# Performance work log

Hardware: AMD Instinct MI355X
Metric: run time of the kernel (lower is better)

## Reference

```python
import jax, jax.numpy as jnp
import numpy as np

B, Q, K, D, H, HD, OUT = 4, 1024, 1024, 256, 8, 32, 256


def setup_inputs() -> dict:
    key = jax.random.key(0)
    ks = jax.random.split(key, 11)
    s = 0.05  # small init scale for weights
    return {
        "q_data": jax.random.normal(ks[0], (B, Q, D), jnp.float32),
        "m_data": jax.random.normal(ks[1], (B, K, D), jnp.float32),
        "bias": jax.random.normal(ks[2], (B, 1, 1, K), jnp.float32),
        "nonbatched_bias": jax.random.normal(ks[3], (H, Q, K), jnp.float32),
        "query_w": jax.random.normal(ks[4], (D, H, HD), jnp.float32) * s,
        "key_w": jax.random.normal(ks[5], (D, H, HD), jnp.float32) * s,
        "value_w": jax.random.normal(ks[6], (D, H, HD), jnp.float32) * s,
        "gating_w": jax.random.normal(ks[7], (D, H, HD), jnp.float32) * s,
        "gating_b": jnp.ones((H, HD), jnp.float32),
        "output_w": jax.random.normal(ks[8], (H, HD, OUT), jnp.float32) * s,
        "output_b": jnp.zeros((OUT,), jnp.float32),
    }


def reference(q_data, m_data, bias, nonbatched_bias, query_w, key_w, value_w,
              gating_w, gating_b, output_w, output_b):
    key_dim = query_w.shape[-1]
    # QKV projections; queries pre-scaled by 1/sqrt(head_dim)
    q = jnp.einsum('bqa,ahc->bqhc', q_data, query_w) * key_dim ** (-0.5)
    k = jnp.einsum('bka,ahc->bkhc', m_data, key_w)
    v = jnp.einsum('bka,ahc->bkhc', m_data, value_w)
    # attention logits [b,h,q,k] plus batched and nonbatched additive biases
    logits_update = jnp.einsum('bqhc,bkhc->bhqk', q, k)
    logits = logits_update + bias + nonbatched_bias[None]
    weights = jax.nn.softmax(logits, axis=-1)
    weighted_avg = jnp.einsum('bhqk,bkhc->bqhc', weights, v)
    # sigmoid gating on the value-aggregated output
    gate = jax.nn.sigmoid(jnp.einsum('bqc,chv->bqhv', q_data, gating_w) + gating_b)
    weighted_avg = weighted_avg * gate
    output = jnp.einsum('bqhc,hco->bqo', weighted_avg, output_w) + output_b
    return (output, logits_update)
```

## Files before the change

### kernel.cpp

```cpp
#include <hip/hip_runtime.h>
#include <hip/hip_bf16.h>

#define NB 4
#define NQ 1024
#define NKS 1024
#define ND 256
#define NH 8
#define NHD 32
#define NOUT 256

typedef __attribute__((ext_vector_type(8))) short v8s;
typedef __attribute__((ext_vector_type(4))) short v4s;
typedef __attribute__((ext_vector_type(4))) float f32x4;

__global__ __launch_bounds__(256) void prep_all(
    const float* __restrict__ qd, const float* __restrict__ md,
    const float* __restrict__ qw, const float* __restrict__ kw,
    const float* __restrict__ vw, const float* __restrict__ gw,
    const float* __restrict__ ow,
    __hip_bfloat16* __restrict__ Abf, __hip_bfloat16* __restrict__ Wt)
{
  if (blockIdx.x < 1024) {
    const int gid = blockIdx.x * 256 + threadIdx.x;
    const float* src = (gid < 131072) ? qd : md;
    const size_t off = (size_t)(gid & 131071) * 8;
    const float4 a = ((const float4*)(src + off))[0];
    const float4 c = ((const float4*)(src + off))[1];
    __hip_bfloat16 t8[8];
    t8[0]=__float2bfloat16(a.x); t8[1]=__float2bfloat16(a.y);
    t8[2]=__float2bfloat16(a.z); t8[3]=__float2bfloat16(a.w);
    t8[4]=__float2bfloat16(c.x); t8[5]=__float2bfloat16(c.y);
    t8[6]=__float2bfloat16(c.z); t8[7]=__float2bfloat16(c.w);
    *(v8s*)(Abf + (size_t)gid * 8) = *(v8s*)t8;
    return;
  }
  __shared__ float tile[64][65];
  const int wb = blockIdx.x - 1024;
  const int m = wb >> 4, bx = wb & 15;
  const float* src = (m == 0) ? qw : (m == 1) ? kw : (m == 2) ? vw
                   : (m == 3) ? gw : ow;
  const float scale = (m == 0) ? 0.1767766952966369f : 1.0f;
  const int d0 = (bx >> 2) * 64, o0 = (bx & 3) * 64;
  #pragma unroll
  for (int i = 0; i < 16; ++i) {
    const int idx = threadIdx.x + i * 256;
    tile[idx >> 6][idx & 63] = src[(size_t)(d0 + (idx >> 6)) * 256 + o0 + (idx & 63)];
  }
  __syncthreads();
  __hip_bfloat16* dst = Wt + (size_t)m * 65536;
  #pragma unroll
  for (int i = 0; i < 16; ++i) {
    const int idx = threadIdx.x + i * 256;
    const int orow = idx >> 6, dc = idx & 63;
    dst[(size_t)(o0 + orow) * 256 + d0 + dc] = __float2bfloat16(tile[dc][orow] * scale);
  }
}

__global__ __launch_bounds__(256) void proj_kernel(
    const __hip_bfloat16* __restrict__ Abf, const __hip_bfloat16* __restrict__ Wt,
    const float* __restrict__ gating_b,
    __hip_bfloat16* __restrict__ Qw, __hip_bfloat16* __restrict__ Kw,
    __hip_bfloat16* __restrict__ Vt, __hip_bfloat16* __restrict__ G)
{
  const int wv = threadIdx.x >> 6, lane = threadIdx.x & 63;
  const int c = lane & 15, g = lane >> 4;
  const int task = blockIdx.x * 4 + wv;
  const int ctg = task & 3;
  const int mat = (task >> 2) & 1;
  const int r0g = (task >> 3) & 255;
  const int src = task >> 11;
  const int r0 = r0g * 16;
  const int b = r0 >> 10, pos0 = r0 & 1023;
  const f32x4 z = {0.f, 0.f, 0.f, 0.f};

  const __hip_bfloat16* A = Abf + ((size_t)src * 4096 + r0) * 256;
  v8s af[8];
  #pragma unroll
  for (int ks = 0; ks < 8; ++ks)
    af[ks] = *(const v8s*)(A + c * 256 + ks * 32 + g * 8);

  const int widx = (src == 0) ? (mat ? 3 : 0) : (mat ? 2 : 1);
  const __hip_bfloat16* W = Wt + (size_t)widx * 65536;
  const bool swapped = (src == 1) && (mat == 1);

  f32x4 ac[4] = {z, z, z, z};
  #pragma unroll
  for (int ks = 0; ks < 8; ++ks) {
    #pragma unroll
    for (int j = 0; j < 4; ++j) {
      v8s wf = *(const v8s*)(W + (size_t)((ctg * 4 + j) * 16 + c) * 256 + ks * 32 + g * 8);
      ac[j] = swapped
        ? __builtin_amdgcn_mfma_f32_16x16x32_bf16(wf, af[ks], ac[j], 0, 0, 0)
        : __builtin_amdgcn_mfma_f32_16x16x32_bf16(af[ks], wf, ac[j], 0, 0, 0);
    }
  }

  if (src == 0 && mat == 0) {
    #pragma unroll
    for (int j = 0; j < 4; ++j) {
      const int o = (ctg * 4 + j) * 16 + c, h = o >> 5, hd = o & 31;
      #pragma unroll
      for (int r = 0; r < 4; ++r)
        Qw[((size_t)(b * NH + h) * 1024 + pos0 + 4 * g + r) * 32 + hd] =
            __float2bfloat16(ac[j][r]);
    }
  } else if (src == 0) {
    #pragma unroll
    for (int j = 0; j < 4; ++j) {
      const int o = (ctg * 4 + j) * 16 + c;
      const float gb = gating_b[o];
      #pragma unroll
      for (int r = 0; r < 4; ++r)
        G[(size_t)(r0 + 4 * g + r) * 256 + o] = __float2bfloat16(ac[j][r] + gb);
    }
  } else if (mat == 0) {
    #pragma unroll
    for (int j = 0; j < 4; ++j) {
      const int o = (ctg * 4 + j) * 16 + c, h = o >> 5, hd = o & 31;
      #pragma unroll
      for (int r = 0; r < 4; ++r)
        Kw[((size_t)(b * NH + h) * 1024 + pos0 + 4 * g + r) * 32 + hd] =
            __float2bfloat16(ac[j][r]);
    }
  } else {
    #pragma unroll
    for (int j = 0; j < 4; ++j) {
      #pragma unroll
      for (int r = 0; r < 4; ++r) {
        const int o2 = (ctg * 4 + j) * 16 + 4 * g + r;
        Vt[((size_t)(b * NH + (o2 >> 5)) * 32 + (o2 & 31)) * 1024 + pos0 + c] =
            __float2bfloat16(ac[j][r]);
      }
    }
  }
}

__global__ __launch_bounds__(256) void attn_kernel(
    const __hip_bfloat16* __restrict__ Qw, const __hip_bfloat16* __restrict__ Kw,
    const __hip_bfloat16* __restrict__ Vt,
    const float* __restrict__ bias, const float* __restrict__ nbb,
    const __hip_bfloat16* __restrict__ G,
    float* __restrict__ out_logits, __hip_bfloat16* __restrict__ WA)
{
  __shared__ __align__(16) __hip_bfloat16 sP[4][16][72];

  const int wv = threadIdx.x >> 6, lane = threadIdx.x & 63;
  const int c = lane & 15, g = lane >> 4;
  const int xcd   = blockIdx.x & 7;
  const int slot  = blockIdx.x >> 3;
  const int bh    = ((slot >> 4) << 3) | xcd;
  const int qtg   = slot & 15;
  const int qt  = qtg * 4 + wv;
  const int b = bh >> 3, h = bh & 7;
  const int q0 = qt * 16;
  const size_t bhs = (size_t)bh;

  const __hip_bfloat16* Kbase = Kw + bhs * NKS * NHD;
  const __hip_bfloat16* Vbase = Vt + bhs * NHD * NKS;
  const float* biasb = bias + (size_t)b * NKS;
  const float* nbbb  = nbb + ((size_t)h * NQ + q0) * NKS;

  const v8s qfrag = *(const v8s*)(Qw + (bhs * NQ + q0 + c) * NHD + g * 8);

  const f32x4 zacc = {0.f, 0.f, 0.f, 0.f};
  f32x4 O0 = zacc, O1 = zacc;
  float lsumL[4] = {0.f, 0.f, 0.f, 0.f};

  auto loadKV = [&](int k0, v8s* kf, v8s* vf) {
    kf[0] = *(const v8s*)(Kbase + (k0 +      c) * NHD + g * 8);
    kf[1] = *(const v8s*)(Kbase + (k0 + 16 + c) * NHD + g * 8);
    kf[2] = *(const v8s*)(Kbase + (k0 + 32 + c) * NHD + g * 8);
    kf[3] = *(const v8s*)(Kbase + (k0 + 48 + c) * NHD + g * 8);
    vf[0] = *(const v8s*)(Vbase + (     c) * NKS + k0 +      g * 8);
    vf[1] = *(const v8s*)(Vbase + (16 + c) * NKS + k0 +      g * 8);
    vf[2] = *(const v8s*)(Vbase + (     c) * NKS + k0 + 32 + g * 8);
    vf[3] = *(const v8s*)(Vbase + (16 + c) * NKS + k0 + 32 + g * 8);
  };
  auto loadBias = [&](int k0, float* bn) {
    #pragma unroll
    for (int t = 0; t < 4; ++t) {
      const float bvt = biasb[k0 + t * 16 + c];
      #pragma unroll
      for (int r = 0; r < 4; ++r)
        bn[t * 4 + r] = bvt + nbbb[(g * 4 + r) * NKS + k0 + t * 16 + c];
    }
  };

  auto compute = [&](int k0, const v8s* kf, const v8s* vf, const float* bn) {
    f32x4 S[4];
    #pragma unroll
    for (int t = 0; t < 4; ++t)
      S[t] = __builtin_amdgcn_mfma_f32_16x16x32_bf16(qfrag, kf[t], zacc, 0, 0, 0);

    #pragma unroll
    for (int r = 0; r < 4; ++r) {
      const int qrow = q0 + g * 4 + r;
      float* lp = out_logits + (bhs * NQ + qrow) * (size_t)NKS + k0 + c;
      float psum = 0.f;
      #pragma unroll
      for (int t = 0; t < 4; ++t) {
        lp[t * 16] = S[t][r];
        const float p = __expf(S[t][r] + bn[t * 4 + r]);
        psum += p;
        sP[wv][g * 4 + r][t * 16 + c] = __float2bfloat16(p);
      }
      lsumL[r] += psum;
    }

    const v8s pa0 = *(const v8s*)&sP[wv][c][g * 8];
    const v8s pa1 = *(const v8s*)&sP[wv][c][32 + g * 8];
    O0 = __builtin_amdgcn_mfma_f32_16x16x32_bf16(pa0, vf[0], O0, 0, 0, 0);
    O0 = __builtin_amdgcn_mfma_f32_16x16x32_bf16(pa1, vf[2], O0, 0, 0, 0);
    O1 = __builtin_amdgcn_mfma_f32_16x16x32_bf16(pa0, vf[1], O1, 0, 0, 0);
    O1 = __builtin_amdgcn_mfma_f32_16x16x32_bf16(pa1, vf[3], O1, 0, 0, 0);
  };

  v8s kfA[4], vfA[4], kfB[4], vfB[4];
  float bnA[16], bnB[16];

  loadKV(0, kfA, vfA);
  loadBias(0, bnA);
  #pragma unroll 1
  for (int kt = 0; kt < NKS / 64; kt += 2) {
    loadKV((kt + 1) * 64, kfB, vfB);
    loadBias((kt + 1) * 64, bnB);
    compute(kt * 64, kfA, vfA, bnA);
    if (kt + 2 < NKS / 64) {
      loadKV((kt + 2) * 64, kfA, vfA);
      loadBias((kt + 2) * 64, bnA);
    }
    compute((kt + 1) * 64, kfB, vfB, bnB);
  }

  #pragma unroll
  for (int r = 0; r < 4; ++r) {
    float rs = lsumL[r];
    rs += __shfl_xor(rs, 1);
    rs += __shfl_xor(rs, 2);
    rs += __shfl_xor(rs, 4);
    rs += __shfl_xor(rs, 8);
    const float inv = 1.0f / rs;
    const int qrow = q0 + g * 4 + r;
    const size_t gb = ((size_t)b * NQ + qrow) * 256 + h * NHD;
    const float gl0 = __bfloat162float(G[gb + c]);
    const float gl1 = __bfloat162float(G[gb + 16 + c]);
    WA[gb + c]      = __float2bfloat16(O0[r] * inv * (1.f / (1.f + __expf(-gl0))));
    WA[gb + 16 + c] = __float2bfloat16(O1[r] * inv * (1.f / (1.f + __expf(-gl1))));
  }
}

__global__ __launch_bounds__(256) void outproj_kernel(
    const __hip_bfloat16* __restrict__ WA, const __hip_bfloat16* __restrict__ WtO,
    const float* __restrict__ output_b, float* __restrict__ out)
{
  const int t = threadIdx.x;
  const int wv = t >> 6, lane = t & 63;
  const int c = lane & 15, g = lane >> 4;
  const int r0 = blockIdx.x * 16;

  const f32x4 z = {0.f, 0.f, 0.f, 0.f};
  f32x4 ac[4] = {z, z, z, z};
  #pragma unroll
  for (int ks = 0; ks < 8; ++ks) {
    const v8s af = *(const v8s*)(WA + (size_t)(r0 + c) * 256 + ks * 32 + g * 8);
    #pragma unroll
    for (int j = 0; j < 4; ++j) {
      const v8s wf = *(const v8s*)(WtO + (size_t)((wv * 4 + j) * 16 + c) * 256 + ks * 32 + g * 8);
      ac[j] = __builtin_amdgcn_mfma_f32_16x16x32_bf16(af, wf, ac[j], 0, 0, 0);
    }
  }
  #pragma unroll
  for (int j = 0; j < 4; ++j) {
    const int o = (wv * 4 + j) * 16 + c;
    const float ob = output_b[o];
    #pragma unroll
    for (int r = 0; r < 4; ++r)
      out[(size_t)(r0 + 4 * g + r) * 256 + o] = ac[j][r] + ob;
  }
}

extern "C" void kernel_launch(void* const* d_in, const int* in_sizes, int n_in,
                              void* d_out, int out_size, void* d_ws, size_t ws_size,
                              hipStream_t stream) {
  const float* q_data   = (const float*)d_in[0];
  const float* m_data   = (const float*)d_in[1];
  const float* bias     = (const float*)d_in[2];
  const float* nbb      = (const float*)d_in[3];
  const float* query_w  = (const float*)d_in[4];
  const float* key_w    = (const float*)d_in[5];
  const float* value_w  = (const float*)d_in[6];
  const float* gating_w = (const float*)d_in[7];
  const float* gating_b = (const float*)d_in[8];
  const float* output_w = (const float*)d_in[9];
  const float* output_b = (const float*)d_in[10];

  float* out        = (float*)d_out;
  float* out_logits = out + (size_t)NB * NQ * NOUT;

  char* ws = (char*)d_ws;
  const size_t MB = 1u << 20;
  __hip_bfloat16* Qw  = (__hip_bfloat16*)(ws);
  __hip_bfloat16* Kw  = (__hip_bfloat16*)(ws + 2 * MB);
  __hip_bfloat16* Vt  = (__hip_bfloat16*)(ws + 4 * MB);
  __hip_bfloat16* G   = (__hip_bfloat16*)(ws + 6 * MB);
  __hip_bfloat16* Abf = (__hip_bfloat16*)(ws + 10 * MB);
  __hip_bfloat16* WA  = (__hip_bfloat16*)(ws + 10 * MB);
  __hip_bfloat16* Wt  = (__hip_bfloat16*)(ws + 20 * MB);

  prep_all<<<1104, 256, 0, stream>>>(q_data, m_data, query_w, key_w, value_w,
                                     gating_w, output_w, Abf, Wt);
  proj_kernel<<<1024, 256, 0, stream>>>(Abf, Wt, gating_b, Qw, Kw, Vt, G);
  attn_kernel<<<512, 256, 0, stream>>>(Qw, Kw, Vt, bias, nbb, G, out_logits, WA);
  outproj_kernel<<<256, 256, 0, stream>>>(WA, Wt + (size_t)4 * 65536, output_b, out);
}
```

Baseline: 77.82 us.

## Fuse fp32-to-bf16 activation conversion into projection kernel via shared memory

The separate pass that converted q_data and m_data to bf16 in global memory is removed. Each projection block now loads its 16 fp32 input rows, converts them, and stages them in LDS, where its four waves share them. The block-to-task mapping changes so one block covers all four column groups of a single row tile and matrix. This avoids writing and re-reading a bf16 activation copy, at the cost of each block re-reading fp32 rows (twice per source, once per matrix) and adding a barrier.

```diff
diff --git a/kernel.cpp b/kernel.cpp
--- a/kernel.cpp
+++ b/kernel.cpp
@@ -13,29 +13,13 @@
 typedef __attribute__((ext_vector_type(4))) short v4s;
 typedef __attribute__((ext_vector_type(4))) float f32x4;
 
-__global__ __launch_bounds__(256) void prep_all(
-    const float* __restrict__ qd, const float* __restrict__ md,
+__global__ __launch_bounds__(256) void prep_w(
     const float* __restrict__ qw, const float* __restrict__ kw,
     const float* __restrict__ vw, const float* __restrict__ gw,
-    const float* __restrict__ ow,
-    __hip_bfloat16* __restrict__ Abf, __hip_bfloat16* __restrict__ Wt)
+    const float* __restrict__ ow, __hip_bfloat16* __restrict__ Wt)
 {
-  if (blockIdx.x < 1024) {
-    const int gid = blockIdx.x * 256 + threadIdx.x;
-    const float* src = (gid < 131072) ? qd : md;
-    const size_t off = (size_t)(gid & 131071) * 8;
-    const float4 a = ((const float4*)(src + off))[0];
-    const float4 c = ((const float4*)(src + off))[1];
-    __hip_bfloat16 t8[8];
-    t8[0]=__float2bfloat16(a.x); t8[1]=__float2bfloat16(a.y);
-    t8[2]=__float2bfloat16(a.z); t8[3]=__float2bfloat16(a.w);
-    t8[4]=__float2bfloat16(c.x); t8[5]=__float2bfloat16(c.y);
-    t8[6]=__float2bfloat16(c.z); t8[7]=__float2bfloat16(c.w);
-    *(v8s*)(Abf + (size_t)gid * 8) = *(v8s*)t8;
-    return;
-  }
   __shared__ float tile[64][65];
-  const int wb = blockIdx.x - 1024;
+  const int wb = blockIdx.x;
   const int m = wb >> 4, bx = wb & 15;
   const float* src = (m == 0) ? qw : (m == 1) ? kw : (m == 2) ? vw
                    : (m == 3) ? gw : ow;
@@ -57,27 +41,41 @@
 }
 
 __global__ __launch_bounds__(256) void proj_kernel(
-    const __hip_bfloat16* __restrict__ Abf, const __hip_bfloat16* __restrict__ Wt,
-    const float* __restrict__ gating_b,
+    const float* __restrict__ qdata, const float* __restrict__ mdata,
+    const __hip_bfloat16* __restrict__ Wt, const float* __restrict__ gating_b,
     __hip_bfloat16* __restrict__ Qw, __hip_bfloat16* __restrict__ Kw,
     __hip_bfloat16* __restrict__ Vt, __hip_bfloat16* __restrict__ G)
 {
+  __shared__ __align__(16) __hip_bfloat16 sA[16][264];
+
   const int wv = threadIdx.x >> 6, lane = threadIdx.x & 63;
   const int c = lane & 15, g = lane >> 4;
-  const int task = blockIdx.x * 4 + wv;
-  const int ctg = task & 3;
-  const int mat = (task >> 2) & 1;
-  const int r0g = (task >> 3) & 255;
-  const int src = task >> 11;
+  const int ctg = wv;
+  const int mat = blockIdx.x & 1;
+  const int r0g = (blockIdx.x >> 1) & 255;
+  const int src = blockIdx.x >> 9;
   const int r0 = r0g * 16;
   const int b = r0 >> 10, pos0 = r0 & 1023;
   const f32x4 z = {0.f, 0.f, 0.f, 0.f};
 
-  const __hip_bfloat16* A = Abf + ((size_t)src * 4096 + r0) * 256;
+  {
+    const float* A = (src ? mdata : qdata) + (size_t)r0 * 256;
+    const int row = threadIdx.x >> 6, col4 = (threadIdx.x & 63) * 4;
+    #pragma unroll
+    for (int i = 0; i < 4; ++i) {
+      const f32x4 a = *(const f32x4*)(A + (size_t)(row + i * 4) * 256 + col4);
+      __hip_bfloat16 t4[4];
+      t4[0] = __float2bfloat16(a.x); t4[1] = __float2bfloat16(a.y);
+      t4[2] = __float2bfloat16(a.z); t4[3] = __float2bfloat16(a.w);
+      *(v4s*)&sA[row + i * 4][col4] = *(v4s*)t4;
+    }
+  }
+  __syncthreads();
+
   v8s af[8];
   #pragma unroll
   for (int ks = 0; ks < 8; ++ks)
-    af[ks] = *(const v8s*)(A + c * 256 + ks * 32 + g * 8);
+    af[ks] = *(const v8s*)&sA[c][ks * 32 + g * 8];
 
   const int widx = (src == 0) ? (mat ? 3 : 0) : (mat ? 2 : 1);
   const __hip_bfloat16* W = Wt + (size_t)widx * 65536;
@@ -303,13 +301,11 @@
   __hip_bfloat16* Kw  = (__hip_bfloat16*)(ws + 2 * MB);
   __hip_bfloat16* Vt  = (__hip_bfloat16*)(ws + 4 * MB);
   __hip_bfloat16* G   = (__hip_bfloat16*)(ws + 6 * MB);
-  __hip_bfloat16* Abf = (__hip_bfloat16*)(ws + 10 * MB);
   __hip_bfloat16* WA  = (__hip_bfloat16*)(ws + 10 * MB);
   __hip_bfloat16* Wt  = (__hip_bfloat16*)(ws + 20 * MB);
 
-  prep_all<<<1104, 256, 0, stream>>>(q_data, m_data, query_w, key_w, value_w,
-                                     gating_w, output_w, Abf, Wt);
-  proj_kernel<<<1024, 256, 0, stream>>>(Abf, Wt, gating_b, Qw, Kw, Vt, G);
+  prep_w<<<80, 256, 0, stream>>>(query_w, key_w, value_w, gating_w, output_w, Wt);
+  proj_kernel<<<1024, 256, 0, stream>>>(q_data, m_data, Wt, gating_b, Qw, Kw, Vt, G);
   attn_kernel<<<512, 256, 0, stream>>>(Qw, Kw, Vt, bias, nbb, G, out_logits, WA);
   outproj_kernel<<<256, 256, 0, stream>>>(WA, Wt + (size_t)4 * 65536, output_b, out);
 }
```

New measurement: 76.26 us (median of 2 runs). 1.02x faster.
